# Kernel optimization log

Measured on AMD Instinct MI355X. Metric: run time of the kernel, lower is better.

## Reference

```python
import jax, jax.numpy as jnp
import numpy as np

B, L, D = 4, 2048, 256
EXPAND, D_STATE, D_CONV = 2, 16, 4
D_INNER = EXPAND * D
DT_RANK = (D + 15) // 16  # ceil(d_model/16) = 16
N_HEADS = 4
H_MLP = int(D * 4.0)
EPS = 1e-5


def _ln(x, w, b):
    mu = x.mean(-1, keepdims=True)
    var = ((x - mu) ** 2).mean(-1, keepdims=True)
    return (x - mu) / jnp.sqrt(var + EPS) * w + b


def _silu(x):
    return x * jax.nn.sigmoid(x)


def _mamba(x, Win, convw, convb, Wx, Wdt, bdt, Alog, Dp, Wout):
    # x: (B, L, D) -> (B, L, D). Standard Mamba mixer (selective scan).
    b, l, d = x.shape
    xz = x @ Win.T                      # (b, l, 2*d_inner)
    xi, z = jnp.split(xz, 2, axis=-1)
    # depthwise causal conv1d, kernel D_CONV
    xc = jnp.swapaxes(xi, 1, 2)         # (b, d_inner, l)
    xc = jax.lax.conv_general_dilated(
        xc, convw, (1,), [(D_CONV - 1, 0)],
        feature_group_count=D_INNER, dimension_numbers=('NCW', 'OIW', 'NCW'))
    xi = _silu(jnp.swapaxes(xc + convb[None, :, None], 1, 2))  # (b, l, d_inner)
    dbl = xi @ Wx.T                     # (b, l, dt_rank + 2*d_state)
    dt = jax.nn.softplus(dbl[..., :DT_RANK] @ Wdt.T + bdt)     # (b, l, d_inner)
    Bm = dbl[..., DT_RANK:DT_RANK + D_STATE]                    # (b, l, n)
    Cm = dbl[..., DT_RANK + D_STATE:]                            # (b, l, n)
    A = -jnp.exp(Alog)                  # (d_inner, n)

    def step(h, ins):
        dt_t, B_t, C_t, u_t = ins       # (b,d_inner),(b,n),(b,n),(b,d_inner)
        h = h * jnp.exp(dt_t[..., None] * A) + dt_t[..., None] * B_t[:, None, :] * u_t[..., None]
        return h, jnp.einsum('bdn,bn->bd', h, C_t)

    xs = tuple(jnp.swapaxes(t, 0, 1) for t in (dt, Bm, Cm, xi))  # time-major
    h0 = jnp.zeros((b, D_INNER, D_STATE), x.dtype)
    _, ys = jax.lax.scan(step, h0, xs)  # ys: (l, b, d_inner)
    y = jnp.swapaxes(ys, 0, 1) + xi * Dp
    return (y * _silu(z)) @ Wout.T


def _attn(x, Wqkv, bqkv, Wo, bo):
    b, l, d = x.shape
    hd = d // N_HEADS
    qkv = x @ Wqkv.T + bqkv
    q, k, v = jnp.split(qkv, 3, axis=-1)
    sh = lambda t: t.reshape(b, l, N_HEADS, hd).transpose(0, 2, 1, 3)
    q, k, v = sh(q), sh(k), sh(v)
    a = jax.nn.softmax(jnp.einsum('bhqd,bhkd->bhqk', q, k) / np.float32(np.sqrt(hd)), axis=-1)
    o = jnp.einsum('bhqk,bhkd->bhqd', a, v).transpose(0, 2, 1, 3).reshape(b, l, d)
    return o @ Wo.T + bo


def setup_inputs() -> dict:
    key = jax.random.key(0)
    ks = iter(jax.random.split(key, 40))
    rn = lambda shape, s=0.02: jax.random.normal(next(ks), shape, jnp.float32) * s
    inp = {'x': jax.random.normal(next(ks), (B, L, D), jnp.float32)}
    for p in ('mf', 'mb'):
        inp[p + '_Win'] = rn((2 * D_INNER, D))
        inp[p + '_convw'] = rn((D_INNER, 1, D_CONV), 0.1)
        inp[p + '_convb'] = jnp.zeros((D_INNER,), jnp.float32)
        inp[p + '_Wx'] = rn((DT_RANK + 2 * D_STATE, D_INNER))
        inp[p + '_Wdt'] = rn((D_INNER, DT_RANK), 0.1)
        inp[p + '_bdt'] = rn((D_INNER,), 0.5)
        inp[p + '_Alog'] = jnp.log(jnp.broadcast_to(jnp.arange(1, D_STATE + 1, dtype=jnp.float32), (D_INNER, D_STATE)))
        inp[p + '_D'] = jnp.ones((D_INNER,), jnp.float32)
        inp[p + '_Wout'] = rn((D, D_INNER))
    for n in ('n1', 'n2', 'n3'):
        inp[n + 'w'] = jnp.ones((D,), jnp.float32)
        inp[n + 'b'] = jnp.zeros((D,), jnp.float32)
    inp['Wqkv'] = rn((3 * D, D))
    inp['bqkv'] = jnp.zeros((3 * D,), jnp.float32)
    inp['Wo'] = rn((D, D))
    inp['bo'] = jnp.zeros((D,), jnp.float32)
    inp['fc1w'] = rn((H_MLP, D))
    inp['fc1b'] = jnp.zeros((H_MLP,), jnp.float32)
    inp['fc2w'] = rn((D, H_MLP))
    inp['fc2b'] = jnp.zeros((D,), jnp.float32)
    return inp


def reference(x, n1w, n1b, n2w, n2b, n3w, n3b,
              mf_Win, mf_convw, mf_convb, mf_Wx, mf_Wdt, mf_bdt, mf_Alog, mf_D, mf_Wout,
              mb_Win, mb_convw, mb_convb, mb_Wx, mb_Wdt, mb_bdt, mb_Alog, mb_D, mb_Wout,
              Wqkv, bqkv, Wo, bo, fc1w, fc1b, fc2w, fc2b):
    # Mamba branch (bidirectional): DropPath is identity at eval
    h = _ln(x, n1w, n1b)
    fwd = _mamba(h, mf_Win, mf_convw, mf_convb, mf_Wx, mf_Wdt, mf_bdt, mf_Alog, mf_D, mf_Wout)
    bwd = jnp.flip(_mamba(jnp.flip(h, 1), mb_Win, mb_convw, mb_convb, mb_Wx, mb_Wdt, mb_bdt, mb_Alog, mb_D, mb_Wout), 1)
    x = x + fwd + bwd
    # Attention branch (full attention since window=None)
    x = x + _attn(_ln(x, n2w, n2b), Wqkv, bqkv, Wo, bo)
    # MLP branch (exact GELU like torch default)
    h = _ln(x, n3w, n3b)
    x = x + (jax.nn.gelu(h @ fc1w.T + fc1b, approximate=False) @ fc2w.T + fc2b)
    return x
```

## Files before the change

### kernel.cpp

```cpp
#include <hip/hip_runtime.h>
#include <hip/hip_bf16.h>
#include <math.h>

#define LL 2048
#define DD 256
#define MTOT 8192
#define DINNER 512
#define CT 32
#define NC 64

typedef __attribute__((ext_vector_type(8))) short short8;
typedef __attribute__((ext_vector_type(4))) float f32x4;

__device__ __forceinline__ float us2f(unsigned short u){
  return __uint_as_float(((unsigned)u) << 16);
}
__device__ __forceinline__ unsigned short f2us(float f){
  __hip_bfloat16 h = __float2bfloat16(f);
  return *(unsigned short*)&h;
}

__global__ void probe_kernel(const unsigned* __restrict__ alog, int* __restrict__ flag){
  if (threadIdx.x == 0 && blockIdx.x == 0) *flag = (alog[0] != 0u) ? 1 : 0;
}

struct Srcs { const void* p[32]; unsigned off[33]; unsigned foff[32]; };

__global__ __launch_bounds__(256) void cvt_all_kernel(Srcs s, float* __restrict__ dst,
                                                      unsigned short* __restrict__ db,
                                                      const int* __restrict__ flag,
                                                      unsigned total){
  unsigned i = blockIdx.x * 256u + threadIdx.x;
  if (i >= total) return;
  int k = 31;
  while (s.off[k] > i) --k;
  unsigned j = i - s.off[k];
  float v;
  if (*flag) v = us2f(((const unsigned short*)s.p[k])[j]);
  else       v = ((const float*)s.p[k])[j];
  if ((k == 24 && j < 65536u) || (k == 25 && j < 256u)) v *= 0.125f;
  db[i] = f2us(v);
  if (s.foff[k] != 0xFFFFFFFFu) dst[s.foff[k] + j] = v;
}

__global__ __launch_bounds__(256) void cvt_x_kernel(const void* __restrict__ src,
                                                    float* __restrict__ dst,
                                                    const int* __restrict__ flag, unsigned n){
  unsigned i = blockIdx.x * 256u + threadIdx.x;
  if (i >= n) return;
  if (*flag) dst[i] = us2f(((const unsigned short*)src)[i]);
  else       dst[i] = ((const float*)src)[i];
}

__global__ __launch_bounds__(256) void wc_prep_kernel(
    const float* __restrict__ Wdt, int dsWdt,
    const float* __restrict__ Wx, int dsWx,
    unsigned short* __restrict__ Wc)
{
  const unsigned g = blockIdx.x * 256u + threadIdx.x;
  const int dir = g >> 18;
  const unsigned idx = g & 262143u;
  const int n = idx >> 9, k = idx & 511;
  const float* wd = Wdt + (size_t)dir * dsWdt + n * 16;
  const float* wx = Wx + (size_t)dir * dsWx + k;
  float s = 0.f;
  #pragma unroll
  for (int j = 0; j < 16; ++j) s = fmaf(wd[j], wx[(size_t)j * 512], s);
  Wc[g] = f2us(s);
}

__global__ __launch_bounds__(256) void final_out_kernel(
    const float* __restrict__ xf, void* __restrict__ out,
    const int* __restrict__ flag, unsigned n)
{
  unsigned i = blockIdx.x * 256u + threadIdx.x;
  if (i >= n) return;
  float v = xf[i];
  if (*flag) ((unsigned short*)out)[i] = f2us(v);
  else       ((float*)out)[i] = v;
}

enum { G_BF16=0, G_GELU=1, G_RESID=2 };
__global__ __launch_bounds__(256) void gemm_mfma_kernel(
    const unsigned short* __restrict__ A, int lda, int agap,
    const unsigned short* __restrict__ W, const unsigned short* __restrict__ W2,
    int Kw, int nsplit, int ksplit,
    const float* __restrict__ bias,
    unsigned short* __restrict__ Cb, float* __restrict__ resid,
    int N, int K, int kslices, int mode)
{
  __shared__ unsigned short sA[64][40];
  __shared__ unsigned short sW[64][40];
  const int tid = threadIdx.x;
  const int w = tid >> 6, lane = tid & 63, quad = lane >> 4, l16 = lane & 15;
  const int m0 = blockIdx.y << 6, n0 = blockIdx.x << 6;
  const int ks = blockIdx.z;
  const int kper = K / kslices;
  const int srow = tid >> 2, skc = (tid & 3) << 3;
  int wr = n0 + srow;
  const unsigned short* Wbase = W;
  if (nsplit && wr >= nsplit){ Wbase = W2; wr -= nsplit; }
  f32x4 acc[4] = {};
  for (int k0 = ks * kper; k0 < ks * kper + kper; k0 += 32){
    int ac = k0 + skc;
    if (agap && ac >= 512) ac += 512;
    short8 av = *(const short8*)(A + (size_t)(m0 + srow) * lda + ac);
    int kk = k0 + skc;
    const unsigned short* Wp = Wbase;
    if (ksplit && kk >= ksplit){ Wp = W2; kk -= ksplit; }
    short8 wv = *(const short8*)(Wp + (size_t)wr * Kw + kk);
    __syncthreads();
    *(short8*)&sA[srow][skc] = av;
    *(short8*)&sW[srow][skc] = wv;
    __syncthreads();
    short8 af = *(const short8*)&sA[w * 16 + l16][quad << 3];
    #pragma unroll
    for (int ns = 0; ns < 4; ++ns){
      short8 wf = *(const short8*)&sW[ns * 16 + l16][quad << 3];
      acc[ns] = __builtin_amdgcn_mfma_f32_16x16x32_bf16(af, wf, acc[ns], 0, 0, 0);
    }
  }
  #pragma unroll
  for (int ns = 0; ns < 4; ++ns){
    const int n = n0 + ns * 16 + l16;
    const float bv = (bias && (mode != G_RESID || ks == 0)) ? bias[n] : 0.f;
    #pragma unroll
    for (int r = 0; r < 4; ++r){
      const int m = m0 + w * 16 + quad * 4 + r;
      const size_t off = (size_t)m * N + n;
      float v = acc[ns][r] + bv;
      if (mode == G_BF16) Cb[off] = f2us(v);
      else if (mode == G_GELU) Cb[off] = f2us(0.5f * v * (1.f + erff(v * 0.70710678118f)));
      else atomicAdd(resid + off, v);
    }
  }
}

__global__ __launch_bounds__(256) void dtbc_mfma_kernel(
    const unsigned short* __restrict__ xi,
    const unsigned short* __restrict__ Wc,
    const unsigned short* __restrict__ WxBCf,
    const unsigned short* __restrict__ WxBCb,
    const float* __restrict__ bdt0, int dsBdt,
    unsigned short* __restrict__ dt16,
    float* __restrict__ dblBC)
{
  __shared__ unsigned short sA[64][40];
  __shared__ unsigned short sW[64][40];
  const int tid = threadIdx.x;
  const int w = tid >> 6, lane = tid & 63, quad = lane >> 4, l16 = lane & 15;
  const int bx = blockIdx.x, m0 = blockIdx.y << 6, dir = blockIdx.z;
  const bool isBC = (bx == 8);
  const unsigned short* A = xi + (size_t)dir * 4194304;
  const unsigned short* W;
  if (isBC) W = dir ? WxBCb : WxBCf;
  else      W = Wc + (size_t)dir * 262144 + ((size_t)bx << 6) * 512;
  const int srow = tid >> 2, skc = (tid & 3) << 3;
  const int wrow = isBC ? (srow & 31) : srow;
  f32x4 acc[4] = {};
  for (int k0 = 0; k0 < 512; k0 += 32){
    short8 av = *(const short8*)(A + (size_t)(m0 + srow) * 512 + k0 + skc);
    short8 wv = *(const short8*)(W + (size_t)wrow * 512 + k0 + skc);
    __syncthreads();
    *(short8*)&sA[srow][skc] = av;
    *(short8*)&sW[srow][skc] = wv;
    __syncthreads();
    short8 af = *(const short8*)&sA[w * 16 + l16][quad << 3];
    #pragma unroll
    for (int ns = 0; ns < 4; ++ns){
      short8 wf = *(const short8*)&sW[ns * 16 + l16][quad << 3];
      acc[ns] = __builtin_amdgcn_mfma_f32_16x16x32_bf16(af, wf, acc[ns], 0, 0, 0);
    }
  }
  #pragma unroll
  for (int ns = 0; ns < 4; ++ns){
    const int nl = ns * 16 + l16;
    #pragma unroll
    for (int r = 0; r < 4; ++r){
      const int m = m0 + w * 16 + quad * 4 + r;
      float v = acc[ns][r];
      if (!isBC){
        const int n = (bx << 6) + nl;
        v += (bdt0 + (size_t)dir * dsBdt)[n];
        float sp = (v > 20.f) ? v : log1pf(__expf(v));
        dt16[(size_t)dir * 4194304 + (size_t)m * 512 + n] = f2us(sp);
      } else if (nl < 32){
        dblBC[(size_t)dir * 262144 + (size_t)m * 32 + nl] = v;
      }
    }
  }
}

__global__ __launch_bounds__(256) void ln_kernel(
    const float* __restrict__ xin,
    const float* __restrict__ w, const float* __restrict__ b,
    unsigned short* __restrict__ hout)
{
  const int row = blockIdx.x, tid = threadIdx.x;
  const size_t off = (size_t)row * DD + tid;
  float v = xin[off];
  float s = v, s2 = v * v;
  #pragma unroll
  for (int o = 32; o; o >>= 1){ s += __shfl_xor(s, o); s2 += __shfl_xor(s2, o); }
  __shared__ float ls[4], ls2[4];
  if ((tid & 63) == 0){ ls[tid >> 6] = s; ls2[tid >> 6] = s2; }
  __syncthreads();
  s  = ls[0] + ls[1] + ls[2] + ls[3];
  s2 = ls2[0] + ls2[1] + ls2[2] + ls2[3];
  const float mu  = s * (1.f / DD);
  const float var = s2 * (1.f / DD) - mu * mu;
  const float inv = rsqrtf(var + 1e-5f);
  hout[off] = f2us((v - mu) * inv * w[tid] + b[tid]);
}

__global__ __launch_bounds__(256) void conv_silu_kernel(
    const unsigned short* __restrict__ xzc, const float* __restrict__ convw0, int dsCw,
    const float* __restrict__ convb0, int dsCb, unsigned short* __restrict__ xi)
{
  const unsigned idx = blockIdx.x * 256u + threadIdx.x;
  const int c = idx & 511;
  const int t = (idx >> 9) & 2047;
  const int b = (idx >> 20) & 3;
  const int dir = idx >> 22;
  const float* cw = convw0 + (size_t)dir * dsCw;
  float acc = (convb0 + (size_t)dir * dsCb)[c];
  if (!dir){
    #pragma unroll
    for (int k = 0; k < 4; ++k){
      int tt = t - 3 + k;
      if (tt >= 0) acc += cw[c*4 + k] * us2f(xzc[((size_t)(b*2048 + tt))*2048 + c]);
    }
  } else {
    #pragma unroll
    for (int j = 0; j < 4; ++j){
      int tt = t + j;
      if (tt < 2048) acc += cw[c*4 + 3 - j] * us2f(xzc[((size_t)(b*2048 + tt))*2048 + 1024 + c]);
    }
  }
  xi[(size_t)dir * 4194304 + ((size_t)(b*2048 + t))*512 + c] = f2us(acc / (1.f + __expf(-acc)));
}

__global__ __launch_bounds__(256) void scan_part1_kernel(
    const unsigned short* __restrict__ dtb, int dsDt,
    const unsigned short* __restrict__ xib, int dsXi,
    const float* __restrict__ dblb, int dsDbl,
    const float* __restrict__ Alog, int dsAl,
    float* __restrict__ dtsum, int dsDts,
    float* __restrict__ hend, int dsHend)
{
  const int bx = blockIdx.x;
  const int dg = bx & 1, c = (bx >> 1) & (NC - 1), b = (bx >> 7) & 3, dir = bx >> 9;
  const int tid = threadIdx.x;
  const int d = dg * 256 + tid;
  const unsigned short* dt_ = dtb + (size_t)dir * dsDt;
  const unsigned short* xi_ = xib + (size_t)dir * dsXi;
  const float* db_ = dblb + (size_t)dir * dsDbl;
  const float* Al_ = Alog + (size_t)dir * dsAl;
  __shared__ float sB[CT][16];
  for (int i = tid; i < CT * 16; i += 256){
    const int s = i >> 4, nn = i & 15;
    const int t = dir ? (LL - 1 - (c * CT + s)) : (c * CT + s);
    sB[s][nn] = db_[(size_t)(b * LL + t) * 32 + nn];
  }
  float A[16];
  #pragma unroll
  for (int n = 0; n < 16; ++n) A[n] = -__expf(Al_[d * 16 + n]);
  __syncthreads();
  float h[16];
  #pragma unroll
  for (int n = 0; n < 16; ++n) h[n] = 0.f;
  float dts = 0.f;
  for (int s = 0; s < CT; ++s){
    const int t = dir ? (LL - 1 - (c * CT + s)) : (c * CT + s);
    const size_t row = (size_t)(b * LL + t);
    const float dtv = us2f(dt_[row * 512 + d]);
    const float uv  = us2f(xi_[row * 512 + d]);
    const float dtu = dtv * uv;
    dts += dtv;
    float bl[16];
    #pragma unroll
    for (int q = 0; q < 4; ++q) *(float4*)&bl[q * 4] = *(const float4*)&sB[s][q * 4];
    #pragma unroll
    for (int n = 0; n < 16; ++n){
      const float e = __expf(dtv * A[n]);
      h[n] = h[n] * e + dtu * bl[n];
    }
  }
  const size_t base = (size_t)dir * dsHend + ((size_t)((b * NC + c) * 512 + d)) * 16;
  #pragma unroll
  for (int q = 0; q < 4; ++q) *(float4*)&hend[base + q * 4] = *(const float4*)&h[q * 4];
  dtsum[(size_t)dir * dsDts + (size_t)(b * NC + c) * 512 + d] = dts;
}

__global__ __launch_bounds__(256) void scan_combine_kernel(
    const float* __restrict__ dtsum, int dsDts,
    float* __restrict__ hend, int dsHend,
    const float* __restrict__ Alog, int dsAl)
{
  const unsigned g = blockIdx.x * 256u + threadIdx.x;
  const int dir = g >> 15;
  const unsigned gg = g & 32767u;
  const int b = gg >> 13, d = (gg >> 4) & 511, n = gg & 15;
  const float A = -__expf((Alog + (size_t)dir * dsAl)[d * 16 + n]);
  const float* dts_ = dtsum + (size_t)dir * dsDts;
  float* he_ = hend + (size_t)dir * dsHend;
  float h = 0.f;
  for (int c = 0; c < NC; ++c){
    const size_t sb = ((size_t)((b * NC + c) * 512 + d)) * 16 + n;
    const float e = __expf(dts_[(size_t)(b * NC + c) * 512 + d] * A);
    const float he = he_[sb];
    he_[sb] = h;
    h = h * e + he;
  }
}

__global__ __launch_bounds__(256) void scan_part2_kernel(
    const unsigned short* __restrict__ dtb, int dsDt,
    const unsigned short* __restrict__ xib, int dsXi,
    const float* __restrict__ dblb, int dsDbl,
    unsigned short* __restrict__ xzc,
    const float* __restrict__ Alog, int dsAl,
    const float* __restrict__ Dp, int dsD,
    const float* __restrict__ hin, int dsHend)
{
  const int bx = blockIdx.x;
  const int dg = bx & 1, c = (bx >> 1) & (NC - 1), b = (bx >> 7) & 3, dir = bx >> 9;
  const int tid = threadIdx.x;
  const int d = dg * 256 + tid;
  const unsigned short* dt_ = dtb + (size_t)dir * dsDt;
  const unsigned short* xi_ = xib + (size_t)dir * dsXi;
  const float* db_ = dblb + (size_t)dir * dsDbl;
  const float* Al_ = Alog + (size_t)dir * dsAl;
  __shared__ float sB[CT][16];
  __shared__ float sC[CT][16];
  for (int i = tid; i < CT * 16; i += 256){
    const int s = i >> 4, nn = i & 15;
    const int t = dir ? (LL - 1 - (c * CT + s)) : (c * CT + s);
    sB[s][nn] = db_[(size_t)(b * LL + t) * 32 + nn];
    sC[s][nn] = db_[(size_t)(b * LL + t) * 32 + 16 + nn];
  }
  float A[16];
  #pragma unroll
  for (int n = 0; n < 16; ++n) A[n] = -__expf(Al_[d * 16 + n]);
  const float Dv = (Dp + (size_t)dir * dsD)[d];
  __syncthreads();
  float h[16];
  const size_t base = (size_t)dir * dsHend + ((size_t)((b * NC + c) * 512 + d)) * 16;
  #pragma unroll
  for (int q = 0; q < 4; ++q) *(float4*)&h[q * 4] = *(const float4*)&hin[base + q * 4];
  for (int s = 0; s < CT; ++s){
    const int t = dir ? (LL - 1 - (c * CT + s)) : (c * CT + s);
    const size_t row = (size_t)(b * LL + t);
    const float dtv = us2f(dt_[row * 512 + d]);
    const float uv  = us2f(xi_[row * 512 + d]);
    const float dtu = dtv * uv;
    float bl[16], cl[16];
    #pragma unroll
    for (int q = 0; q < 4; ++q){
      *(float4*)&bl[q * 4] = *(const float4*)&sB[s][q * 4];
      *(float4*)&cl[q * 4] = *(const float4*)&sC[s][q * 4];
    }
    float p = uv * Dv;
    #pragma unroll
    for (int n = 0; n < 16; ++n){
      const float e = __expf(dtv * A[n]);
      h[n] = h[n] * e + dtu * bl[n];
      p = fmaf(h[n], cl[n], p);
    }
    const float z = us2f(xzc[row * 2048 + dir * 1024 + 512 + d]);
    xzc[row * 2048 + dir * 1024 + d] = f2us(p * (z / (1.f + __expf(-z))));
  }
}

__global__ __launch_bounds__(256) void v_prep_kernel(
    const unsigned short* __restrict__ qkvb, unsigned short* __restrict__ Vt)
{
  const int kt = blockIdx.x;
  const int bh = blockIdx.y;
  const int b = bh >> 2, h = bh & 3;
  __shared__ unsigned short tile[64][72];
  #pragma unroll
  for (int rr = 0; rr < 4; ++rr){
    const int idx = (rr * 256 + threadIdx.x) * 4;
    const int key = idx >> 6, d = idx & 63;
    ushort4 v = *(const ushort4*)(qkvb + ((size_t)(b * 2048 + kt * 64 + key)) * 768 + 512 + h * 64 + d);
    *(ushort4*)&tile[key][d] = v;
  }
  __syncthreads();
  #pragma unroll
  for (int rr = 0; rr < 8; ++rr){
    const int o2 = rr * 256 + threadIdx.x;
    const int d = o2 >> 5, k2 = (o2 & 31) << 1;
    ushort2 u;
    u.x = tile[k2][d];
    u.y = tile[k2 + 1][d];
    *(ushort2*)(Vt + (size_t)bh * 131072 + (size_t)d * 2048 + kt * 64 + k2) = u;
  }
}

__global__ __launch_bounds__(256) void attn_mfma_kernel(
    const unsigned short* __restrict__ qkvb, const unsigned short* __restrict__ Vt,
    float* __restrict__ opart, float* __restrict__ lpart)
{
  __shared__ unsigned short sK[64][72];
  __shared__ unsigned short sV[64][72];
  __shared__ unsigned short sP[4][16][72];
  const int tid = threadIdx.x;
  const int w = tid >> 6, lane = tid & 63, quad = lane >> 4, l16 = lane & 15;
  const int bh = blockIdx.y;
  const int b = bh >> 2, h = bh & 3;
  const int q0 = blockIdx.x * 64;
  const int split = blockIdx.z;

  const unsigned short* qp = qkvb + ((size_t)(b * 2048 + q0 + w * 16 + l16)) * 768 + h * 64 + quad * 8;
  short8 qf0 = *(const short8*)qp;
  short8 qf1 = *(const short8*)(qp + 32);

  f32x4 o[4] = {{0,0,0,0},{0,0,0,0},{0,0,0,0},{0,0,0,0}};
  float lsum[4] = {0.f,0.f,0.f,0.f};

  const int kt0 = split * 1024;
  for (int kt = kt0; kt < kt0 + 1024; kt += 64){
    __syncthreads();
    #pragma unroll
    for (int r = 0; r < 2; ++r){
      const int idx = (r * 256 + tid) * 8;
      const int row = idx >> 6, c = idx & 63;
      *(short8*)&sK[row][c] = *(const short8*)(qkvb + ((size_t)(b * 2048 + kt + row)) * 768 + 256 + h * 64 + c);
      *(short8*)&sV[row][c] = *(const short8*)(Vt + (size_t)bh * 131072 + (size_t)row * 2048 + kt + c);
    }
    __syncthreads();

    float p[4][4];
    #pragma unroll
    for (int sub = 0; sub < 4; ++sub){
      short8 bk0 = *(const short8*)&sK[sub * 16 + l16][quad * 8];
      short8 bk1 = *(const short8*)&sK[sub * 16 + l16][32 + quad * 8];
      f32x4 acc = {0,0,0,0};
      acc = __builtin_amdgcn_mfma_f32_16x16x32_bf16(qf0, bk0, acc, 0, 0, 0);
      acc = __builtin_amdgcn_mfma_f32_16x16x32_bf16(qf1, bk1, acc, 0, 0, 0);
      #pragma unroll
      for (int r = 0; r < 4; ++r) p[sub][r] = __expf(acc[r]);
    }
    #pragma unroll
    for (int r = 0; r < 4; ++r)
      lsum[r] += p[0][r] + p[1][r] + p[2][r] + p[3][r];
    #pragma unroll
    for (int sub = 0; sub < 4; ++sub)
      #pragma unroll
      for (int r = 0; r < 4; ++r)
        sP[w][quad * 4 + r][sub * 16 + l16] = f2us(p[sub][r]);
    short8 pa0 = *(const short8*)&sP[w][l16][quad * 8];
    short8 pa1 = *(const short8*)&sP[w][l16][32 + quad * 8];
    #pragma unroll
    for (int nsub = 0; nsub < 4; ++nsub){
      short8 bv0 = *(const short8*)&sV[nsub * 16 + l16][quad * 8];
      short8 bv1 = *(const short8*)&sV[nsub * 16 + l16][32 + quad * 8];
      o[nsub] = __builtin_amdgcn_mfma_f32_16x16x32_bf16(pa0, bv0, o[nsub], 0, 0, 0);
      o[nsub] = __builtin_amdgcn_mfma_f32_16x16x32_bf16(pa1, bv1, o[nsub], 0, 0, 0);
    }
  }

  #pragma unroll
  for (int r = 0; r < 4; ++r){
    lsum[r] += __shfl_xor(lsum[r], 1); lsum[r] += __shfl_xor(lsum[r], 2);
    lsum[r] += __shfl_xor(lsum[r], 4); lsum[r] += __shfl_xor(lsum[r], 8);
  }
  const size_t obase = ((size_t)(split * 16 + bh)) * 2048;
  #pragma unroll
  for (int r = 0; r < 4; ++r){
    const int q = q0 + w * 16 + quad * 4 + r;
    #pragma unroll
    for (int nsub = 0; nsub < 4; ++nsub)
      opart[(obase + q) * 64 + nsub * 16 + l16] = o[nsub][r];
    if (l16 == 0) lpart[obase + q] = lsum[r];
  }
}

__global__ __launch_bounds__(256) void attn_merge_kernel(
    const float* __restrict__ opart, const float* __restrict__ lpart,
    unsigned short* __restrict__ outp)
{
  const unsigned g = blockIdx.x * 256u + threadIdx.x;
  const int d4 = (g & 15) << 2;
  const int q = (g >> 4) & 2047;
  const int bh = g >> 15;
  const size_t i0 = ((size_t)bh * 2048 + q) * 64 + d4;
  const size_t i1 = i0 + (size_t)16 * 2048 * 64;
  float4 o0 = *(const float4*)(opart + i0);
  float4 o1 = *(const float4*)(opart + i1);
  const float invl = 1.f / (lpart[bh * 2048 + q] + lpart[16 * 2048 + bh * 2048 + q]);
  const int b = bh >> 2, h = bh & 3;
  ushort4 u;
  u.x = f2us((o0.x + o1.x) * invl);
  u.y = f2us((o0.y + o1.y) * invl);
  u.z = f2us((o0.z + o1.z) * invl);
  u.w = f2us((o0.w + o1.w) * invl);
  *(ushort4*)(outp + ((size_t)(b * 2048 + q)) * 256 + h * 64 + d4) = u;
}

extern "C" void kernel_launch(void* const* d_in, const int* in_sizes, int n_in,
                              void* d_out, int out_size, void* d_ws, size_t ws_size,
                              hipStream_t stream)
{
  static const bool needf[33] = {
    false, false,true,true,true,true,true,true,true,false,
    false,true,true,true,true,true,true,true,false,
    true,true,true,true,true,true,
    false,true,false,true,false,true,false,true };

  int* flag  = (int*)d_ws;
  float* wts = (float*)d_ws + 16;

  Srcs srcs;
  unsigned acc = 0, facc = 0;
  unsigned foff_h[33];
  for (int i = 1; i <= 32; ++i){
    srcs.p[i - 1] = d_in[i];
    srcs.off[i - 1] = acc;
    acc += (unsigned)in_sizes[i];
    if (needf[i]){ srcs.foff[i - 1] = facc; foff_h[i] = facc; facc += (unsigned)in_sizes[i]; }
    else { srcs.foff[i - 1] = 0xFFFFFFFFu; foff_h[i] = 0xFFFFFFFFu; }
  }
  srcs.off[32] = acc;
  const unsigned wtotal = acc;
  const unsigned ftot = (facc + 3u) & ~3u;

  unsigned short* wb16 = (unsigned short*)(wts + ftot);
  float* xf    = wts + ftot + (wtotal + 1) / 2;
  float* xzc_f = xf + 2097152;
  float* xi_f  = xzc_f + 8388608;
  float* dblBC = xi_f + 4194304;
  float* hb_f  = dblBC + 524288;
  float* dt_f  = hb_f + 1048576;
  float* hend  = dt_f + 4194304;
  float* dtsum = hend + 4194304;
  float* wc_f  = dtsum + 262144;

  unsigned short* xzc  = (unsigned short*)xzc_f;
  unsigned short* xi16 = (unsigned short*)xi_f;
  unsigned short* hb16 = (unsigned short*)hb_f;
  unsigned short* dt16 = (unsigned short*)dt_f;
  unsigned short* Wc16 = (unsigned short*)wc_f;
  unsigned short* qkvb = xzc;
  unsigned short* Vt   = (unsigned short*)hend;
  float* opart = xi_f;
  float* lpart = dtsum;
  unsigned short* fc1o = xzc;

  auto wp  = [&](int i){ return wts + foff_h[i]; };
  auto wp16= [&](int i){ return wb16 + srcs.off[i - 1]; };

  hipLaunchKernelGGL(probe_kernel, dim3(1), dim3(64), 0, stream,
      (const unsigned*)d_in[7], flag);
  hipLaunchKernelGGL(cvt_all_kernel, dim3((wtotal + 255) / 256), dim3(256), 0, stream,
      srcs, wts, wb16, flag, wtotal);
  hipLaunchKernelGGL(cvt_x_kernel, dim3(MTOT * DD / 256), dim3(256), 0, stream,
      d_in[0], xf, flag, (unsigned)(MTOT * DD));

  const int dsCw = (int)(foff_h[11] - foff_h[2]);
  const int dsAl = (int)(foff_h[16] - foff_h[7]);
  const int dsD  = (int)(foff_h[17] - foff_h[8]);
  const int dsWx = (int)(foff_h[13] - foff_h[4]);
  const int dsWdt= (int)(foff_h[14] - foff_h[5]);
  const int dsBdt= (int)(foff_h[15] - foff_h[6]);
  const int dsCb2= (int)(foff_h[12] - foff_h[3]);

  hipLaunchKernelGGL(wc_prep_kernel, dim3(2048), dim3(256), 0, stream,
      wp(5), dsWdt, wp(4), dsWx, Wc16);

  auto gemm16 = [&](const unsigned short* Ab, int lda, int agap,
                    const unsigned short* W, const unsigned short* W2,
                    int Kw, int nsplit, int ksplit, const float* bias,
                    unsigned short* Cb, float* resid,
                    int N, int K, int ksl, int mode){
    hipLaunchKernelGGL(gemm_mfma_kernel, dim3(N / 64, MTOT / 64, ksl), dim3(256), 0, stream,
        Ab, lda, agap, W, W2, Kw, nsplit, ksplit, bias, Cb, resid, N, K, ksl, mode);
  };

  hipLaunchKernelGGL(ln_kernel, dim3(MTOT), dim3(256), 0, stream,
      xf, wp(19), wp(20), hb16);

  gemm16(hb16, 256, 0, wp16(1), wp16(10), 256, 1024, 0, nullptr,
         xzc, nullptr, 2048, 256, 1, G_BF16);
  hipLaunchKernelGGL(conv_silu_kernel, dim3(2 * MTOT * DINNER / 256), dim3(256), 0, stream,
      xzc, wp(2), dsCw, wp(3), dsCb2, xi16);
  hipLaunchKernelGGL(dtbc_mfma_kernel, dim3(9, MTOT / 64, 2), dim3(256), 0, stream,
      xi16, Wc16, wp16(4) + 8192, wp16(13) + 8192, wp(6), dsBdt, dt16, dblBC);
  hipLaunchKernelGGL(scan_part1_kernel, dim3(1024), dim3(256), 0, stream,
      dt16, 4194304, xi16, 4194304, dblBC, 262144, wp(7), dsAl,
      dtsum, 131072, hend, 2097152);
  hipLaunchKernelGGL(scan_combine_kernel, dim3(256), dim3(256), 0, stream,
      dtsum, 131072, hend, 2097152, wp(7), dsAl);
  hipLaunchKernelGGL(scan_part2_kernel, dim3(1024), dim3(256), 0, stream,
      dt16, 4194304, xi16, 4194304, dblBC, 262144, xzc, wp(7), dsAl,
      wp(8), dsD, hend, 2097152);
  gemm16(xzc, 2048, 1, wp16(9), wp16(18), 512, 0, 512, nullptr,
         nullptr, xf, 256, 1024, 2, G_RESID);

  hipLaunchKernelGGL(ln_kernel, dim3(MTOT), dim3(256), 0, stream,
      xf, wp(21), wp(22), hb16);
  gemm16(hb16, 256, 0, wp16(25), nullptr, 256, 0, 0, wp(26),
         qkvb, nullptr, 768, 256, 1, G_BF16);
  hipLaunchKernelGGL(v_prep_kernel, dim3(32, 16), dim3(256), 0, stream,
      qkvb, Vt);
  hipLaunchKernelGGL(attn_mfma_kernel, dim3(32, 16, 2), dim3(256), 0, stream,
      qkvb, Vt, opart, lpart);
  hipLaunchKernelGGL(attn_merge_kernel, dim3(2048), dim3(256), 0, stream,
      opart, lpart, hb16);
  gemm16(hb16, 256, 0, wp16(27), nullptr, 256, 0, 0, wp(28),
         nullptr, xf, 256, 256, 2, G_RESID);

  hipLaunchKernelGGL(ln_kernel, dim3(MTOT), dim3(256), 0, stream,
      xf, wp(23), wp(24), hb16);
  gemm16(hb16, 256, 0, wp16(29), nullptr, 256, 0, 0, wp(30),
         fc1o, nullptr, 1024, 256, 1, G_GELU);
  gemm16(fc1o, 1024, 0, wp16(31), nullptr, 1024, 0, 0, wp(32),
         nullptr, xf, 256, 1024, 2, G_RESID);
  hipLaunchKernelGGL(final_out_kernel, dim3(MTOT * DD / 256), dim3(256), 0, stream,
      xf, d_out, flag, (unsigned)(MTOT * DD));
}
```

Measured before the change: 513.5 us.

## Use direct global-to-LDS loads in dtbc GEMM and split attention keys four ways

The dt/B/C projection GEMM now stages tiles with global_load_lds (direct global-to-LDS DMA) into an XOR-swizzled, unpadded LDS layout, instead of loading through registers and storing to padded arrays. The aim is to drop the register round trip and keep LDS reads free of bank conflicts. Attention is split four ways along the key axis instead of two, with partial outputs placed in two workspace regions and a merge that sums four partials. This gives more blocks for occupancy on the attention pass, at the cost of extra partial-output traffic in the merge.

```diff
diff --git a/kernel.cpp b/kernel.cpp
--- a/kernel.cpp
+++ b/kernel.cpp
@@ -11,6 +11,8 @@
 
 typedef __attribute__((ext_vector_type(8))) short short8;
 typedef __attribute__((ext_vector_type(4))) float f32x4;
+typedef const unsigned __attribute__((address_space(1)))* gas1;
+typedef unsigned __attribute__((address_space(3)))* las3;
 
 __device__ __forceinline__ float us2f(unsigned short u){
   return __uint_as_float(((unsigned)u) << 16);
@@ -145,30 +147,35 @@
     unsigned short* __restrict__ dt16,
     float* __restrict__ dblBC)
 {
-  __shared__ unsigned short sA[64][40];
-  __shared__ unsigned short sW[64][40];
+  __shared__ unsigned short sA[2048];
+  __shared__ unsigned short sW[2048];
   const int tid = threadIdx.x;
   const int w = tid >> 6, lane = tid & 63, quad = lane >> 4, l16 = lane & 15;
   const int bx = blockIdx.x, m0 = blockIdx.y << 6, dir = blockIdx.z;
   const bool isBC = (bx == 8);
-  const unsigned short* A = xi + (size_t)dir * 4194304;
-  const unsigned short* W;
-  if (isBC) W = dir ? WxBCb : WxBCf;
-  else      W = Wc + (size_t)dir * 262144 + ((size_t)bx << 6) * 512;
-  const int srow = tid >> 2, skc = (tid & 3) << 3;
-  const int wrow = isBC ? (srow & 31) : srow;
+  const unsigned short* Wt;
+  if (isBC) Wt = dir ? WxBCb : WxBCf;
+  else      Wt = Wc + (size_t)dir * 262144 + ((size_t)bx << 6) * 512;
+  const int r = tid >> 2;
+  const int cblk = ((tid & 3) - (r >> 1)) & 3;
+  const int ccol = cblk << 3;
+  const unsigned short* Arow = xi + (size_t)dir * 4194304 + (size_t)(m0 + r) * 512;
+  const unsigned short* Wrow = Wt + (size_t)(isBC ? (r & 31) : r) * 512;
+  las3 ldsA = (las3)(void*)(sA + (w << 9));
+  las3 ldsW = (las3)(void*)(sW + (w << 9));
+  const int ra = w * 16 + l16;
+  const int offA = ra * 32 + (((quad + (ra >> 1)) & 3) << 3);
   f32x4 acc[4] = {};
   for (int k0 = 0; k0 < 512; k0 += 32){
-    short8 av = *(const short8*)(A + (size_t)(m0 + srow) * 512 + k0 + skc);
-    short8 wv = *(const short8*)(W + (size_t)wrow * 512 + k0 + skc);
     __syncthreads();
-    *(short8*)&sA[srow][skc] = av;
-    *(short8*)&sW[srow][skc] = wv;
+    __builtin_amdgcn_global_load_lds((gas1)(const void*)(Arow + k0 + ccol), ldsA, 16, 0, 0);
+    __builtin_amdgcn_global_load_lds((gas1)(const void*)(Wrow + k0 + ccol), ldsW, 16, 0, 0);
     __syncthreads();
-    short8 af = *(const short8*)&sA[w * 16 + l16][quad << 3];
+    short8 af = *(const short8*)(sA + offA);
     #pragma unroll
     for (int ns = 0; ns < 4; ++ns){
-      short8 wf = *(const short8*)&sW[ns * 16 + l16][quad << 3];
+      const int rw = ns * 16 + l16;
+      short8 wf = *(const short8*)(sW + rw * 32 + (((quad + (rw >> 1)) & 3) << 3));
       acc[ns] = __builtin_amdgcn_mfma_f32_16x16x32_bf16(af, wf, acc[ns], 0, 0, 0);
     }
   }
@@ -176,9 +183,9 @@
   for (int ns = 0; ns < 4; ++ns){
     const int nl = ns * 16 + l16;
     #pragma unroll
-    for (int r = 0; r < 4; ++r){
-      const int m = m0 + w * 16 + quad * 4 + r;
-      float v = acc[ns][r];
+    for (int rr = 0; rr < 4; ++rr){
+      const int m = m0 + w * 16 + quad * 4 + rr;
+      float v = acc[ns][rr];
       if (!isBC){
         const int n = (bx << 6) + nl;
         v += (bdt0 + (size_t)dir * dsBdt)[n];
@@ -400,7 +407,7 @@
 
 __global__ __launch_bounds__(256) void attn_mfma_kernel(
     const unsigned short* __restrict__ qkvb, const unsigned short* __restrict__ Vt,
-    float* __restrict__ opart, float* __restrict__ lpart)
+    float* __restrict__ op0, float* __restrict__ op1, float* __restrict__ lpart)
 {
   __shared__ unsigned short sK[64][72];
   __shared__ unsigned short sV[64][72];
@@ -419,8 +426,8 @@
   f32x4 o[4] = {{0,0,0,0},{0,0,0,0},{0,0,0,0},{0,0,0,0}};
   float lsum[4] = {0.f,0.f,0.f,0.f};
 
-  const int kt0 = split * 1024;
-  for (int kt = kt0; kt < kt0 + 1024; kt += 64){
+  const int kt0 = split * 512;
+  for (int kt = kt0; kt < kt0 + 512; kt += 64){
     __syncthreads();
     #pragma unroll
     for (int r = 0; r < 2; ++r){
@@ -466,36 +473,41 @@
     lsum[r] += __shfl_xor(lsum[r], 1); lsum[r] += __shfl_xor(lsum[r], 2);
     lsum[r] += __shfl_xor(lsum[r], 4); lsum[r] += __shfl_xor(lsum[r], 8);
   }
-  const size_t obase = ((size_t)(split * 16 + bh)) * 2048;
+  float* op = (split < 2 ? op0 : op1) + (size_t)(split & 1) * 2097152;
   #pragma unroll
   for (int r = 0; r < 4; ++r){
     const int q = q0 + w * 16 + quad * 4 + r;
     #pragma unroll
     for (int nsub = 0; nsub < 4; ++nsub)
-      opart[(obase + q) * 64 + nsub * 16 + l16] = o[nsub][r];
-    if (l16 == 0) lpart[obase + q] = lsum[r];
+      op[((size_t)bh * 2048 + q) * 64 + nsub * 16 + l16] = o[nsub][r];
+    if (l16 == 0) lpart[(split * 16 + bh) * 2048 + q] = lsum[r];
   }
 }
 
 __global__ __launch_bounds__(256) void attn_merge_kernel(
-    const float* __restrict__ opart, const float* __restrict__ lpart,
-    unsigned short* __restrict__ outp)
+    const float* __restrict__ op0, const float* __restrict__ op1,
+    const float* __restrict__ lpart, unsigned short* __restrict__ outp)
 {
   const unsigned g = blockIdx.x * 256u + threadIdx.x;
   const int d4 = (g & 15) << 2;
   const int q = (g >> 4) & 2047;
   const int bh = g >> 15;
-  const size_t i0 = ((size_t)bh * 2048 + q) * 64 + d4;
-  const size_t i1 = i0 + (size_t)16 * 2048 * 64;
-  float4 o0 = *(const float4*)(opart + i0);
-  float4 o1 = *(const float4*)(opart + i1);
-  const float invl = 1.f / (lpart[bh * 2048 + q] + lpart[16 * 2048 + bh * 2048 + q]);
+  float4 s = make_float4(0.f, 0.f, 0.f, 0.f);
+  float l = 0.f;
+  #pragma unroll
+  for (int sp = 0; sp < 4; ++sp){
+    const float* op = (sp < 2 ? op0 : op1) + (size_t)(sp & 1) * 2097152;
+    float4 o = *(const float4*)(op + ((size_t)bh * 2048 + q) * 64 + d4);
+    s.x += o.x; s.y += o.y; s.z += o.z; s.w += o.w;
+    l += lpart[(sp * 16 + bh) * 2048 + q];
+  }
+  const float invl = 1.f / l;
   const int b = bh >> 2, h = bh & 3;
   ushort4 u;
-  u.x = f2us((o0.x + o1.x) * invl);
-  u.y = f2us((o0.y + o1.y) * invl);
-  u.z = f2us((o0.z + o1.z) * invl);
-  u.w = f2us((o0.w + o1.w) * invl);
+  u.x = f2us(s.x * invl);
+  u.y = f2us(s.y * invl);
+  u.z = f2us(s.z * invl);
+  u.w = f2us(s.w * invl);
   *(ushort4*)(outp + ((size_t)(b * 2048 + q)) * 256 + h * 64 + d4) = u;
 }
 
@@ -544,7 +556,8 @@
   unsigned short* Wc16 = (unsigned short*)wc_f;
   unsigned short* qkvb = xzc;
   unsigned short* Vt   = (unsigned short*)hend;
-  float* opart = xi_f;
+  float* op0   = xzc_f + 4194304;
+  float* op1   = xi_f;
   float* lpart = dtsum;
   unsigned short* fc1o = xzc;
 
@@ -604,10 +617,10 @@
          qkvb, nullptr, 768, 256, 1, G_BF16);
   hipLaunchKernelGGL(v_prep_kernel, dim3(32, 16), dim3(256), 0, stream,
       qkvb, Vt);
-  hipLaunchKernelGGL(attn_mfma_kernel, dim3(32, 16, 2), dim3(256), 0, stream,
-      qkvb, Vt, opart, lpart);
+  hipLaunchKernelGGL(attn_mfma_kernel, dim3(32, 16, 4), dim3(256), 0, stream,
+      qkvb, Vt, op0, op1, lpart);
   hipLaunchKernelGGL(attn_merge_kernel, dim3(2048), dim3(256), 0, stream,
-      opart, lpart, hb16);
+      op0, op1, lpart, hb16);
   gemm16(hb16, 256, 0, wp16(27), nullptr, 256, 0, 0, wp(28),
          nullptr, xf, 256, 256, 2, G_RESID);
 
```

Result: no change. 516.9 us (+0.7%).
